# Performance work log

Hardware: AMD Instinct MI355X
Metric: run time of the kernel (lower is better)

## Reference

```python
import jax, jax.numpy as jnp
import numpy as np

V, D, H, S, W, OUT = 100000, 200, 50, 128, 64, 5

def setup_inputs() -> dict:
    key = jax.random.key(0)
    ks = jax.random.split(key, 24)
    def p(k, shape, scale=0.05):
        return jax.random.normal(k, shape, dtype=jnp.float32) * scale
    return {
        "doc": jax.random.randint(ks[0], (S, W), 0, V),
        "emb": p(ks[1], (V, D), 0.1),
        "w_word": p(ks[2], (H, D)), "b_word": p(ks[3], (H,)),
        "conv_w1": p(ks[4], (H, H, 1)), "conv_b1": p(ks[5], (H,)),
        "conv_w2": p(ks[6], (H, H, 2)), "conv_b2": p(ks[7], (H,)),
        "conv_w3": p(ks[8], (H, H, 3)), "conv_b3": p(ks[9], (H,)),
        "Wi": p(ks[10], (H, H)), "Ui": p(ks[11], (H, H)), "bi": p(ks[12], (H,)),
        "Wf": p(ks[13], (H, H)), "Uf": p(ks[14], (H, H)), "bf": p(ks[15], (H,)),
        "Wr": p(ks[16], (H, H)), "Ur": p(ks[17], (H, H)), "br": p(ks[18], (H,)),
        "W_out": p(ks[19], (OUT, H)), "b_out": p(ks[20], (OUT,)),
    }

def reference(doc, emb, w_word, b_word, conv_w1, conv_b1, conv_w2, conv_b2,
              conv_w3, conv_b3, Wi, Ui, bi, Wf, Uf, bf, Wr, Ur, br, W_out, b_out):
    # Batched word projection: replaces the per-word nn.Linear loop.
    x = emb[doc]                                              # [S, W, D]
    x = jnp.einsum('swd,hd->shw', x, w_word) + b_word[None, :, None]  # [S, H, W]

    def branch(w, b):
        # Conv1d(H, H, k, valid) over time, full-width avg-pool, then tanh
        y = jax.lax.conv_general_dilated(x, w, (1,), 'VALID',
                                         dimension_numbers=('NCH', 'OIH', 'NCH'))
        return jnp.tanh(y.mean(-1) + b)                        # [S, H]

    # mean over the 3 kernel-size branches (conv_result.mean(0) in torch)
    reps = (branch(conv_w1, conv_b1) + branch(conv_w2, conv_b2)
            + branch(conv_w3, conv_b3)) / 3.0                  # [S, H]

    def cell(h, s):
        # GRNN gate (Tang et al. 2015 document GNN)
        i = jax.nn.sigmoid(s @ Wi.T + h @ Ui.T + bi)
        f = jax.nn.sigmoid(s @ Wf.T + h @ Uf.T + bf)
        g = jnp.tanh(s @ Wr.T + h @ Ur.T + br)
        h_new = jnp.tanh(i * g + f * h)
        return h_new, h_new

    h0 = jnp.zeros((H,), dtype=reps.dtype)
    h_last, _ = jax.lax.scan(cell, h0, reps)                   # GnnOutput.LAST
    return jax.nn.softmax(h_last @ W_out.T + b_out)            # [OUT]
```

## Files before the change

### kernel.cpp

```cpp
#include <hip/hip_runtime.h>
#include <cmath>

#define S_   128
#define W_   64
#define D_   200
#define H_   50
#define OUT_ 5

__global__ __launch_bounds__(256) void k_sent(
    const int* __restrict__ doc, const float* __restrict__ emb,
    const float* __restrict__ w_word, const float* __restrict__ b_word,
    const float* __restrict__ cw1, const float* __restrict__ cb1,
    const float* __restrict__ cw2, const float* __restrict__ cb2,
    const float* __restrict__ cw3, const float* __restrict__ cb3,
    const float* __restrict__ Wi, const float* __restrict__ bi,
    const float* __restrict__ Wf, const float* __restrict__ bf,
    const float* __restrict__ Wr, const float* __restrict__ br,
    float* __restrict__ Xout)
{
    const int s   = blockIdx.x;
    const int tid = threadIdx.x;

    __shared__ int   drow[W_];
    __shared__ float vec[5][D_];
    __shared__ float q[5][H_];
    __shared__ float m[6][H_ + 2];
    __shared__ float reps_sh[H_];

    if (tid < W_) drow[tid] = doc[s * W_ + tid];
    __syncthreads();

    if (tid < D_) {
        const int d = tid;
        float acc = 0.f;
        for (int u = 0; u < W_; ++u)
            acc += emb[(size_t)drow[u] * D_ + d];
        vec[0][d] = acc;
        vec[1][d] = emb[(size_t)drow[0]      * D_ + d];
        vec[2][d] = emb[(size_t)drow[1]      * D_ + d];
        vec[3][d] = emb[(size_t)drow[W_ - 2] * D_ + d];
        vec[4][d] = emb[(size_t)drow[W_ - 1] * D_ + d];
    }
    __syncthreads();

    if (tid < 5 * H_) {
        const int v = tid / H_, h = tid % H_;
        const float* wr = w_word + h * D_;
        float acc = 0.f;
        for (int d = 0; d < D_; ++d) acc += wr[d] * vec[v][d];
        q[v][h] = acc;
    }
    __syncthreads();

    if (tid < H_) {
        const int h = tid;
        const float qf = q[0][h], q0 = q[1][h], q1 = q[2][h],
                    q62 = q[3][h], q63 = q[4][h];
        const float bw = b_word[h];
        m[0][h] = qf               * (1.f / 64.f) + bw;
        m[1][h] = (qf - q63)       * (1.f / 63.f) + bw;
        m[2][h] = (qf - q0)        * (1.f / 63.f) + bw;
        m[3][h] = (qf - q62 - q63) * (1.f / 62.f) + bw;
        m[4][h] = (qf - q0  - q63) * (1.f / 62.f) + bw;
        m[5][h] = (qf - q0  - q1)  * (1.f / 62.f) + bw;
    }
    __syncthreads();

    if (tid < H_) {
        const int o = tid;
        float a1 = cb1[o], a2 = cb2[o], a3 = cb3[o];
        for (int i = 0; i < H_; ++i) {
            a1 += cw1[o * H_ + i] * m[0][i];
            const float* c2 = cw2 + (o * H_ + i) * 2;
            a2 += c2[0] * m[1][i] + c2[1] * m[2][i];
            const float* c3 = cw3 + (o * H_ + i) * 3;
            a3 += c3[0] * m[3][i] + c3[1] * m[4][i] + c3[2] * m[5][i];
        }
        reps_sh[o] = (tanhf(a1) + tanhf(a2) + tanhf(a3)) * (1.f / 3.f);
    }
    __syncthreads();

    if (tid < 3 * H_) {
        const int g = tid / H_, o = tid % H_;
        const float* Wg = (g == 0) ? Wi : (g == 1) ? Wf : Wr;
        const float* bg = (g == 0) ? bi : (g == 1) ? bf : br;
        float acc = bg[o];
        for (int j = 0; j < H_; ++j) acc += Wg[o * H_ + j] * reps_sh[j];
        Xout[(g * S_ + s) * H_ + o] = acc;
    }
}

#define JW 13

__device__ __forceinline__ float rcp_fast(float x) {
    return __builtin_amdgcn_rcpf(x);
}

__device__ __forceinline__ float tanh_fast(float x) {
    float e = __expf(2.f * x);
    return (e - 1.f) * rcp_fast(e + 1.f);
}

__device__ __forceinline__ float sigmoid_fast(float x) {
    return rcp_fast(1.f + __expf(-x));
}

__device__ __forceinline__ float bcast(float v, int lane) {
    return __int_as_float(__builtin_amdgcn_readlane(__float_as_int(v), lane));
}

__device__ __forceinline__ void barrier_lds_only() {
    asm volatile("s_waitcnt lgkmcnt(0)" ::: "memory");
    __builtin_amdgcn_s_barrier();
    __builtin_amdgcn_sched_barrier(0);
}

__global__ __launch_bounds__(256, 1) void k_scan(
    const float* __restrict__ X,
    const float* __restrict__ Ui, const float* __restrict__ Uf,
    const float* __restrict__ Ur,
    const float* __restrict__ Wout, const float* __restrict__ bout,
    float* __restrict__ out)
{
    const int tid = threadIdx.x;
    const int w   = tid >> 6;
    const int o   = tid & 63;
    const int ro  = (o < H_) ? o : (H_ - 1);
    const int jlo = w * JW;

    __shared__ float part[2][3][64][5];

    float ua[JW], ub[JW], uc[JW];
    {
        const float* Uir = Ui + ro * H_;
        const float* Ufr = Uf + ro * H_;
        const float* Urr = Ur + ro * H_;
        #pragma unroll
        for (int jj = 0; jj < JW; ++jj) {
            const int j = jlo + jj;
            const bool ok = (j < H_);
            ua[jj] = ok ? Uir[j] : 0.f;
            ub[jj] = ok ? Ufr[j] : 0.f;
            uc[jj] = ok ? Urr[j] : 0.f;
        }
    }

    float h  = 0.f;
    float xi = X[(0 * S_ + 0) * H_ + ro];
    float xf = X[(1 * S_ + 0) * H_ + ro];
    float xr = X[(2 * S_ + 0) * H_ + ro];

    int p = 0;
    for (int t = 0; t < S_; ++t) {
        const int tn = (t + 1 < S_) ? (t + 1) : (S_ - 1);
        float nxi = X[(0 * S_ + tn) * H_ + ro];
        float nxf = X[(1 * S_ + tn) * H_ + ro];
        float nxr = X[(2 * S_ + tn) * H_ + ro];

        float hj[JW];
        #pragma unroll
        for (int jj = 0; jj < JW; ++jj) {
            const int j  = jlo + jj;
            const int jl = (j < H_) ? j : (H_ - 1);
            hj[jj] = bcast(h, jl);
        }

        float pi0 = 0.f, pi1 = 0.f, pf0 = 0.f, pf1 = 0.f,
              pr0 = 0.f, pr1 = 0.f;
        #pragma unroll
        for (int jj = 0; jj + 1 < JW; jj += 2) {
            pi0 += ua[jj]     * hj[jj];
            pf0 += ub[jj]     * hj[jj];
            pr0 += uc[jj]     * hj[jj];
            pi1 += ua[jj + 1] * hj[jj + 1];
            pf1 += ub[jj + 1] * hj[jj + 1];
            pr1 += uc[jj + 1] * hj[jj + 1];
        }
        pi0 += ua[JW - 1] * hj[JW - 1];
        pf0 += ub[JW - 1] * hj[JW - 1];
        pr0 += uc[JW - 1] * hj[JW - 1];

        part[p][0][o][w] = pi0 + pi1;
        part[p][1][o][w] = pf0 + pf1;
        part[p][2][o][w] = pr0 + pr1;
        barrier_lds_only();

        float ai = xi + (part[p][0][o][0] + part[p][0][o][1])
                      + (part[p][0][o][2] + part[p][0][o][3]);
        float af = xf + (part[p][1][o][0] + part[p][1][o][1])
                      + (part[p][1][o][2] + part[p][1][o][3]);
        float ar = xr + (part[p][2][o][0] + part[p][2][o][1])
                      + (part[p][2][o][2] + part[p][2][o][3]);

        float gi = sigmoid_fast(ai);
        float gf = sigmoid_fast(af);
        float gg = tanh_fast(ar);
        h = tanh_fast(gi * gg + gf * h);

        xi = nxi; xf = nxf; xr = nxr;
        p ^= 1;
    }

    float logit = (o < OUT_) ? bout[o] : 0.f;
    const float* wrow = Wout + ((o < OUT_) ? o : 0) * H_;
    #pragma unroll
    for (int j = 0; j < H_; ++j) {
        float hj = bcast(h, j);
        logit += wrow[j] * hj;
    }
    float l0 = bcast(logit, 0), l1 = bcast(logit, 1), l2 = bcast(logit, 2),
          l3 = bcast(logit, 3), l4 = bcast(logit, 4);
    float mx = fmaxf(fmaxf(fmaxf(l0, l1), fmaxf(l2, l3)), l4);
    float e0 = __expf(l0 - mx), e1 = __expf(l1 - mx), e2 = __expf(l2 - mx),
          e3 = __expf(l3 - mx), e4 = __expf(l4 - mx);
    float s = e0 + e1 + e2 + e3 + e4;
    if (tid == 0) {
        float rs = 1.f / s;
        out[0] = e0 * rs; out[1] = e1 * rs; out[2] = e2 * rs;
        out[3] = e3 * rs; out[4] = e4 * rs;
    }
}

extern "C" void kernel_launch(void* const* d_in, const int* in_sizes, int n_in,
                              void* d_out, int out_size, void* d_ws, size_t ws_size,
                              hipStream_t stream) {
    (void)in_sizes; (void)n_in; (void)out_size; (void)ws_size;

    const int*   doc    = (const int*)  d_in[0];
    const float* emb    = (const float*)d_in[1];
    const float* w_word = (const float*)d_in[2];
    const float* b_word = (const float*)d_in[3];
    const float* cw1    = (const float*)d_in[4];
    const float* cb1    = (const float*)d_in[5];
    const float* cw2    = (const float*)d_in[6];
    const float* cb2    = (const float*)d_in[7];
    const float* cw3    = (const float*)d_in[8];
    const float* cb3    = (const float*)d_in[9];
    const float* Wi     = (const float*)d_in[10];
    const float* Ui     = (const float*)d_in[11];
    const float* bi     = (const float*)d_in[12];
    const float* Wf     = (const float*)d_in[13];
    const float* Uf     = (const float*)d_in[14];
    const float* bf     = (const float*)d_in[15];
    const float* Wr     = (const float*)d_in[16];
    const float* Ur     = (const float*)d_in[17];
    const float* br     = (const float*)d_in[18];
    const float* Wout   = (const float*)d_in[19];
    const float* bout   = (const float*)d_in[20];

    float* X = (float*)d_ws;
    float* out = (float*)d_out;

    k_sent<<<S_, 256, 0, stream>>>(doc, emb, w_word, b_word,
                                   cw1, cb1, cw2, cb2, cw3, cb3,
                                   Wi, bi, Wf, bf, Wr, br, X);
    k_scan<<<1, 256, 0, stream>>>(X, Ui, Uf, Ur, Wout, bout, out);
}
```

Baseline: 68.21 us.

## Fuse sentence encoder and GRNN scan into one cooperative kernel with grid sync

Merges the per-sentence encoder kernel and the single-block recurrent scan into one kernel launched cooperatively over 128 blocks. A grid-wide sync separates the two phases, and block 0 then runs the scan. The goal is to remove the second kernel launch and the inter-kernel gap. The cost is the cooperative launch path plus the grid barrier, and the scan block keeps the shared memory of both phases.

```diff
diff --git a/kernel.cpp b/kernel.cpp
--- a/kernel.cpp
+++ b/kernel.cpp
@@ -1,13 +1,36 @@
 #include <hip/hip_runtime.h>
+#include <hip/hip_cooperative_groups.h>
 #include <cmath>
+
+namespace cg = cooperative_groups;
 
 #define S_   128
 #define W_   64
 #define D_   200
 #define H_   50
 #define OUT_ 5
-
-__global__ __launch_bounds__(256) void k_sent(
+#define JW   13
+
+__device__ __forceinline__ float rcp_fast(float x) {
+    return __builtin_amdgcn_rcpf(x);
+}
+__device__ __forceinline__ float tanh_fast(float x) {
+    float e = __expf(2.f * x);
+    return (e - 1.f) * rcp_fast(e + 1.f);
+}
+__device__ __forceinline__ float sigmoid_fast(float x) {
+    return rcp_fast(1.f + __expf(-x));
+}
+__device__ __forceinline__ float bcast(float v, int lane) {
+    return __int_as_float(__builtin_amdgcn_readlane(__float_as_int(v), lane));
+}
+__device__ __forceinline__ void barrier_lds_only() {
+    asm volatile("s_waitcnt lgkmcnt(0)" ::: "memory");
+    __builtin_amdgcn_s_barrier();
+    __builtin_amdgcn_sched_barrier(0);
+}
+
+__global__ __launch_bounds__(256, 1) void k_fused(
     const int* __restrict__ doc, const float* __restrict__ emb,
     const float* __restrict__ w_word, const float* __restrict__ b_word,
     const float* __restrict__ cw1, const float* __restrict__ cb1,
@@ -16,208 +39,189 @@
     const float* __restrict__ Wi, const float* __restrict__ bi,
     const float* __restrict__ Wf, const float* __restrict__ bf,
     const float* __restrict__ Wr, const float* __restrict__ br,
-    float* __restrict__ Xout)
-{
-    const int s   = blockIdx.x;
-    const int tid = threadIdx.x;
-
-    __shared__ int   drow[W_];
-    __shared__ float vec[5][D_];
-    __shared__ float q[5][H_];
-    __shared__ float m[6][H_ + 2];
-    __shared__ float reps_sh[H_];
-
-    if (tid < W_) drow[tid] = doc[s * W_ + tid];
-    __syncthreads();
-
-    if (tid < D_) {
-        const int d = tid;
-        float acc = 0.f;
-        for (int u = 0; u < W_; ++u)
-            acc += emb[(size_t)drow[u] * D_ + d];
-        vec[0][d] = acc;
-        vec[1][d] = emb[(size_t)drow[0]      * D_ + d];
-        vec[2][d] = emb[(size_t)drow[1]      * D_ + d];
-        vec[3][d] = emb[(size_t)drow[W_ - 2] * D_ + d];
-        vec[4][d] = emb[(size_t)drow[W_ - 1] * D_ + d];
-    }
-    __syncthreads();
-
-    if (tid < 5 * H_) {
-        const int v = tid / H_, h = tid % H_;
-        const float* wr = w_word + h * D_;
-        float acc = 0.f;
-        for (int d = 0; d < D_; ++d) acc += wr[d] * vec[v][d];
-        q[v][h] = acc;
-    }
-    __syncthreads();
-
-    if (tid < H_) {
-        const int h = tid;
-        const float qf = q[0][h], q0 = q[1][h], q1 = q[2][h],
-                    q62 = q[3][h], q63 = q[4][h];
-        const float bw = b_word[h];
-        m[0][h] = qf               * (1.f / 64.f) + bw;
-        m[1][h] = (qf - q63)       * (1.f / 63.f) + bw;
-        m[2][h] = (qf - q0)        * (1.f / 63.f) + bw;
-        m[3][h] = (qf - q62 - q63) * (1.f / 62.f) + bw;
-        m[4][h] = (qf - q0  - q63) * (1.f / 62.f) + bw;
-        m[5][h] = (qf - q0  - q1)  * (1.f / 62.f) + bw;
-    }
-    __syncthreads();
-
-    if (tid < H_) {
-        const int o = tid;
-        float a1 = cb1[o], a2 = cb2[o], a3 = cb3[o];
-        for (int i = 0; i < H_; ++i) {
-            a1 += cw1[o * H_ + i] * m[0][i];
-            const float* c2 = cw2 + (o * H_ + i) * 2;
-            a2 += c2[0] * m[1][i] + c2[1] * m[2][i];
-            const float* c3 = cw3 + (o * H_ + i) * 3;
-            a3 += c3[0] * m[3][i] + c3[1] * m[4][i] + c3[2] * m[5][i];
-        }
-        reps_sh[o] = (tanhf(a1) + tanhf(a2) + tanhf(a3)) * (1.f / 3.f);
-    }
-    __syncthreads();
-
-    if (tid < 3 * H_) {
-        const int g = tid / H_, o = tid % H_;
-        const float* Wg = (g == 0) ? Wi : (g == 1) ? Wf : Wr;
-        const float* bg = (g == 0) ? bi : (g == 1) ? bf : br;
-        float acc = bg[o];
-        for (int j = 0; j < H_; ++j) acc += Wg[o * H_ + j] * reps_sh[j];
-        Xout[(g * S_ + s) * H_ + o] = acc;
-    }
-}
-
-#define JW 13
-
-__device__ __forceinline__ float rcp_fast(float x) {
-    return __builtin_amdgcn_rcpf(x);
-}
-
-__device__ __forceinline__ float tanh_fast(float x) {
-    float e = __expf(2.f * x);
-    return (e - 1.f) * rcp_fast(e + 1.f);
-}
-
-__device__ __forceinline__ float sigmoid_fast(float x) {
-    return rcp_fast(1.f + __expf(-x));
-}
-
-__device__ __forceinline__ float bcast(float v, int lane) {
-    return __int_as_float(__builtin_amdgcn_readlane(__float_as_int(v), lane));
-}
-
-__device__ __forceinline__ void barrier_lds_only() {
-    asm volatile("s_waitcnt lgkmcnt(0)" ::: "memory");
-    __builtin_amdgcn_s_barrier();
-    __builtin_amdgcn_sched_barrier(0);
-}
-
-__global__ __launch_bounds__(256, 1) void k_scan(
-    const float* __restrict__ X,
     const float* __restrict__ Ui, const float* __restrict__ Uf,
     const float* __restrict__ Ur,
     const float* __restrict__ Wout, const float* __restrict__ bout,
+    float* __restrict__ X,
     float* __restrict__ out)
 {
     const int tid = threadIdx.x;
-    const int w   = tid >> 6;
-    const int o   = tid & 63;
-    const int ro  = (o < H_) ? o : (H_ - 1);
-    const int jlo = w * JW;
-
-    __shared__ float part[2][3][64][5];
-
-    float ua[JW], ub[JW], uc[JW];
+
     {
-        const float* Uir = Ui + ro * H_;
-        const float* Ufr = Uf + ro * H_;
-        const float* Urr = Ur + ro * H_;
+        const int s = blockIdx.x;
+
+        __shared__ int   drow[W_];
+        __shared__ float vec[5][D_];
+        __shared__ float q[5][H_];
+        __shared__ float m[6][H_ + 2];
+        __shared__ float reps_sh[H_];
+
+        if (tid < W_) drow[tid] = doc[s * W_ + tid];
+        __syncthreads();
+
+        if (tid < D_) {
+            const int d = tid;
+            float acc = 0.f;
+            for (int u = 0; u < W_; ++u)
+                acc += emb[(size_t)drow[u] * D_ + d];
+            vec[0][d] = acc;
+            vec[1][d] = emb[(size_t)drow[0]      * D_ + d];
+            vec[2][d] = emb[(size_t)drow[1]      * D_ + d];
+            vec[3][d] = emb[(size_t)drow[W_ - 2] * D_ + d];
+            vec[4][d] = emb[(size_t)drow[W_ - 1] * D_ + d];
+        }
+        __syncthreads();
+
+        if (tid < 5 * H_) {
+            const int v = tid / H_, h = tid % H_;
+            const float* wr = w_word + h * D_;
+            float acc = 0.f;
+            for (int d = 0; d < D_; ++d) acc += wr[d] * vec[v][d];
+            q[v][h] = acc;
+        }
+        __syncthreads();
+
+        if (tid < H_) {
+            const int h = tid;
+            const float qf = q[0][h], q0 = q[1][h], q1 = q[2][h],
+                        q62 = q[3][h], q63 = q[4][h];
+            const float bw = b_word[h];
+            m[0][h] = qf               * (1.f / 64.f) + bw;
+            m[1][h] = (qf - q63)       * (1.f / 63.f) + bw;
+            m[2][h] = (qf - q0)        * (1.f / 63.f) + bw;
+            m[3][h] = (qf - q62 - q63) * (1.f / 62.f) + bw;
+            m[4][h] = (qf - q0  - q63) * (1.f / 62.f) + bw;
+            m[5][h] = (qf - q0  - q1)  * (1.f / 62.f) + bw;
+        }
+        __syncthreads();
+
+        if (tid < H_) {
+            const int o = tid;
+            float a1 = cb1[o], a2 = cb2[o], a3 = cb3[o];
+            for (int i = 0; i < H_; ++i) {
+                a1 += cw1[o * H_ + i] * m[0][i];
+                const float* c2 = cw2 + (o * H_ + i) * 2;
+                a2 += c2[0] * m[1][i] + c2[1] * m[2][i];
+                const float* c3 = cw3 + (o * H_ + i) * 3;
+                a3 += c3[0] * m[3][i] + c3[1] * m[4][i] + c3[2] * m[5][i];
+            }
+            reps_sh[o] = (tanhf(a1) + tanhf(a2) + tanhf(a3)) * (1.f / 3.f);
+        }
+        __syncthreads();
+
+        if (tid < 3 * H_) {
+            const int g = tid / H_, o = tid % H_;
+            const float* Wg = (g == 0) ? Wi : (g == 1) ? Wf : Wr;
+            const float* bg = (g == 0) ? bi : (g == 1) ? bf : br;
+            float acc = bg[o];
+            for (int j = 0; j < H_; ++j) acc += Wg[o * H_ + j] * reps_sh[j];
+            X[(g * S_ + s) * H_ + o] = acc;
+        }
+        __threadfence();
+    }
+
+    cg::this_grid().sync();
+
+    if (blockIdx.x != 0) return;
+    {
+        const int w   = tid >> 6;
+        const int o   = tid & 63;
+        const int ro  = (o < H_) ? o : (H_ - 1);
+        const int jlo = w * JW;
+
+        __shared__ float part[2][3][64][5];
+
+        float ua[JW], ub[JW], uc[JW];
+        {
+            const float* Uir = Ui + ro * H_;
+            const float* Ufr = Uf + ro * H_;
+            const float* Urr = Ur + ro * H_;
+            #pragma unroll
+            for (int jj = 0; jj < JW; ++jj) {
+                const int j = jlo + jj;
+                const bool ok = (j < H_);
+                ua[jj] = ok ? Uir[j] : 0.f;
+                ub[jj] = ok ? Ufr[j] : 0.f;
+                uc[jj] = ok ? Urr[j] : 0.f;
+            }
+        }
+
+        float h  = 0.f;
+        float xi = X[(0 * S_ + 0) * H_ + ro];
+        float xf = X[(1 * S_ + 0) * H_ + ro];
+        float xr = X[(2 * S_ + 0) * H_ + ro];
+
+        int p = 0;
+        for (int t = 0; t < S_; ++t) {
+            const int tn = (t + 1 < S_) ? (t + 1) : (S_ - 1);
+            float nxi = X[(0 * S_ + tn) * H_ + ro];
+            float nxf = X[(1 * S_ + tn) * H_ + ro];
+            float nxr = X[(2 * S_ + tn) * H_ + ro];
+
+            float hj[JW];
+            #pragma unroll
+            for (int jj = 0; jj < JW; ++jj) {
+                const int j  = jlo + jj;
+                const int jl = (j < H_) ? j : (H_ - 1);
+                hj[jj] = bcast(h, jl);
+            }
+
+            float pi0 = 0.f, pi1 = 0.f, pf0 = 0.f, pf1 = 0.f,
+                  pr0 = 0.f, pr1 = 0.f;
+            #pragma unroll
+            for (int jj = 0; jj + 1 < JW; jj += 2) {
+                pi0 += ua[jj]     * hj[jj];
+                pf0 += ub[jj]     * hj[jj];
+                pr0 += uc[jj]     * hj[jj];
+                pi1 += ua[jj + 1] * hj[jj + 1];
+                pf1 += ub[jj + 1] * hj[jj + 1];
+                pr1 += uc[jj + 1] * hj[jj + 1];
+            }
+            pi0 += ua[JW - 1] * hj[JW - 1];
+            pf0 += ub[JW - 1] * hj[JW - 1];
+            pr0 += uc[JW - 1] * hj[JW - 1];
+
+            part[p][0][o][w] = pi0 + pi1;
+            part[p][1][o][w] = pf0 + pf1;
+            part[p][2][o][w] = pr0 + pr1;
+            barrier_lds_only();
+
+            float ai = xi + (part[p][0][o][0] + part[p][0][o][1])
+                          + (part[p][0][o][2] + part[p][0][o][3]);
+            float af = xf + (part[p][1][o][0] + part[p][1][o][1])
+                          + (part[p][1][o][2] + part[p][1][o][3]);
+            float ar = xr + (part[p][2][o][0] + part[p][2][o][1])
+                          + (part[p][2][o][2] + part[p][2][o][3]);
+
+            float gi = sigmoid_fast(ai);
+            float gf = sigmoid_fast(af);
+            float gg = tanh_fast(ar);
+            h = tanh_fast(gi * gg + gf * h);
+
+            xi = nxi; xf = nxf; xr = nxr;
+            p ^= 1;
+        }
+
+        float logit = (o < OUT_) ? bout[o] : 0.f;
+        const float* wrow = Wout + ((o < OUT_) ? o : 0) * H_;
         #pragma unroll
-        for (int jj = 0; jj < JW; ++jj) {
-            const int j = jlo + jj;
-            const bool ok = (j < H_);
-            ua[jj] = ok ? Uir[j] : 0.f;
-            ub[jj] = ok ? Ufr[j] : 0.f;
-            uc[jj] = ok ? Urr[j] : 0.f;
-        }
-    }
-
-    float h  = 0.f;
-    float xi = X[(0 * S_ + 0) * H_ + ro];
-    float xf = X[(1 * S_ + 0) * H_ + ro];
-    float xr = X[(2 * S_ + 0) * H_ + ro];
-
-    int p = 0;
-    for (int t = 0; t < S_; ++t) {
-        const int tn = (t + 1 < S_) ? (t + 1) : (S_ - 1);
-        float nxi = X[(0 * S_ + tn) * H_ + ro];
-        float nxf = X[(1 * S_ + tn) * H_ + ro];
-        float nxr = X[(2 * S_ + tn) * H_ + ro];
-
-        float hj[JW];
-        #pragma unroll
-        for (int jj = 0; jj < JW; ++jj) {
-            const int j  = jlo + jj;
-            const int jl = (j < H_) ? j : (H_ - 1);
-            hj[jj] = bcast(h, jl);
-        }
-
-        float pi0 = 0.f, pi1 = 0.f, pf0 = 0.f, pf1 = 0.f,
-              pr0 = 0.f, pr1 = 0.f;
-        #pragma unroll
-        for (int jj = 0; jj + 1 < JW; jj += 2) {
-            pi0 += ua[jj]     * hj[jj];
-            pf0 += ub[jj]     * hj[jj];
-            pr0 += uc[jj]     * hj[jj];
-            pi1 += ua[jj + 1] * hj[jj + 1];
-            pf1 += ub[jj + 1] * hj[jj + 1];
-            pr1 += uc[jj + 1] * hj[jj + 1];
-        }
-        pi0 += ua[JW - 1] * hj[JW - 1];
-        pf0 += ub[JW - 1] * hj[JW - 1];
-        pr0 += uc[JW - 1] * hj[JW - 1];
-
-        part[p][0][o][w] = pi0 + pi1;
-        part[p][1][o][w] = pf0 + pf1;
-        part[p][2][o][w] = pr0 + pr1;
-        barrier_lds_only();
-
-        float ai = xi + (part[p][0][o][0] + part[p][0][o][1])
-                      + (part[p][0][o][2] + part[p][0][o][3]);
-        float af = xf + (part[p][1][o][0] + part[p][1][o][1])
-                      + (part[p][1][o][2] + part[p][1][o][3]);
-        float ar = xr + (part[p][2][o][0] + part[p][2][o][1])
-                      + (part[p][2][o][2] + part[p][2][o][3]);
-
-        float gi = sigmoid_fast(ai);
-        float gf = sigmoid_fast(af);
-        float gg = tanh_fast(ar);
-        h = tanh_fast(gi * gg + gf * h);
-
-        xi = nxi; xf = nxf; xr = nxr;
-        p ^= 1;
-    }
-
-    float logit = (o < OUT_) ? bout[o] : 0.f;
-    const float* wrow = Wout + ((o < OUT_) ? o : 0) * H_;
-    #pragma unroll
-    for (int j = 0; j < H_; ++j) {
-        float hj = bcast(h, j);
-        logit += wrow[j] * hj;
-    }
-    float l0 = bcast(logit, 0), l1 = bcast(logit, 1), l2 = bcast(logit, 2),
-          l3 = bcast(logit, 3), l4 = bcast(logit, 4);
-    float mx = fmaxf(fmaxf(fmaxf(l0, l1), fmaxf(l2, l3)), l4);
-    float e0 = __expf(l0 - mx), e1 = __expf(l1 - mx), e2 = __expf(l2 - mx),
-          e3 = __expf(l3 - mx), e4 = __expf(l4 - mx);
-    float s = e0 + e1 + e2 + e3 + e4;
-    if (tid == 0) {
-        float rs = 1.f / s;
-        out[0] = e0 * rs; out[1] = e1 * rs; out[2] = e2 * rs;
-        out[3] = e3 * rs; out[4] = e4 * rs;
+        for (int j = 0; j < H_; ++j) {
+            float hj = bcast(h, j);
+            logit += wrow[j] * hj;
+        }
+        float l0 = bcast(logit, 0), l1 = bcast(logit, 1),
+              l2 = bcast(logit, 2), l3 = bcast(logit, 3),
+              l4 = bcast(logit, 4);
+        float mx = fmaxf(fmaxf(fmaxf(l0, l1), fmaxf(l2, l3)), l4);
+        float e0 = __expf(l0 - mx), e1 = __expf(l1 - mx),
+              e2 = __expf(l2 - mx), e3 = __expf(l3 - mx),
+              e4 = __expf(l4 - mx);
+        float s = e0 + e1 + e2 + e3 + e4;
+        if (tid == 0) {
+            float rs = 1.f / s;
+            out[0] = e0 * rs; out[1] = e1 * rs; out[2] = e2 * rs;
+            out[3] = e3 * rs; out[4] = e4 * rs;
+        }
     }
 }
 
@@ -248,11 +252,17 @@
     const float* Wout   = (const float*)d_in[19];
     const float* bout   = (const float*)d_in[20];
 
-    float* X = (float*)d_ws;
+    float* X   = (float*)d_ws;
     float* out = (float*)d_out;
 
-    k_sent<<<S_, 256, 0, stream>>>(doc, emb, w_word, b_word,
-                                   cw1, cb1, cw2, cb2, cw3, cb3,
-                                   Wi, bi, Wf, bf, Wr, br, X);
-    k_scan<<<1, 256, 0, stream>>>(X, Ui, Uf, Ur, Wout, bout, out);
-}
+    void* args[] = {
+        (void*)&doc, (void*)&emb, (void*)&w_word, (void*)&b_word,
+        (void*)&cw1, (void*)&cb1, (void*)&cw2, (void*)&cb2,
+        (void*)&cw3, (void*)&cb3, (void*)&Wi, (void*)&bi,
+        (void*)&Wf, (void*)&bf, (void*)&Wr, (void*)&br,
+        (void*)&Ui, (void*)&Uf, (void*)&Ur,
+        (void*)&Wout, (void*)&bout, (void*)&X, (void*)&out
+    };
+    hipLaunchCooperativeKernel((const void*)k_fused, dim3(S_), dim3(256),
+                               args, 0, stream);
+}
```

Result: slower. 103.7 us (+52.1%).
